# Performance work log

Measured on AMD Instinct MI355X. Metric: run time of the kernel, lower is better.

Reference implementation:

```python
import jax, jax.numpy as jnp
import numpy as np

D_MODEL = 128
D_STATE = 16
D_CONV = 2
EXPAND = 2
D_INNER = EXPAND * D_MODEL  # 256
DT_RANK = (D_MODEL + 15) // 16  # 8
GROUPS = 4
EPS = 1e-5


def setup_inputs() -> dict:
    key = jax.random.key(0)
    ks = jax.random.split(key, 12)
    s = lambda k, shape, sc=0.02: jax.random.normal(k, shape, dtype=jnp.float32) * sc
    inp = {
        "x_hsi": jax.random.normal(ks[0], (8, D_MODEL, 64, 64), dtype=jnp.float32),
        "W_in": s(ks[1], (D_MODEL, 2 * D_INNER)),            # in_proj (no bias)
        "conv_w": s(ks[2], (D_INNER, D_CONV), 0.5),          # depthwise causal conv, k=2
        "conv_b": s(ks[3], (D_INNER,), 0.1),
        "W_x": s(ks[4], (D_INNER, DT_RANK + 2 * D_STATE)),   # x_proj (no bias)
        "W_dt": s(ks[5], (DT_RANK, D_INNER), 0.1),
        "b_dt": s(ks[6], (D_INNER,), 0.1),
        "A_log": jnp.log(jnp.broadcast_to(jnp.arange(1, D_STATE + 1, dtype=jnp.float32), (D_INNER, D_STATE))),
        "D": jnp.ones((D_INNER,), dtype=jnp.float32),
        "W_out": s(ks[7], (D_INNER, D_MODEL)),               # out_proj (no bias)
        "gn_gamma": jnp.ones((D_MODEL,), dtype=jnp.float32),
        "gn_beta": jnp.zeros((D_MODEL,), dtype=jnp.float32),
    }
    return inp


def _causal_conv_k2(x, w, b):
    # x: [B, L, Din]; w: [Din, 2]; causal depthwise conv, kernel size 2
    xp = jnp.pad(x, ((0, 0), (1, 0), (0, 0)))
    return xp[:, :-1] * w[:, 0] + xp[:, 1:] * w[:, 1] + b


def _selective_scan(xc, dt, Bmat, Cmat, A, D):
    # xc,dt: [B,L,Din]; Bmat,Cmat: [B,L,N]; A: [Din,N]; D: [Din]
    def step(h, inp):
        dt_t, B_t, C_t, x_t = inp          # [B,Din],[B,N],[B,N],[B,Din]
        dA = jnp.exp(dt_t[..., None] * A)                      # [B,Din,N]
        dBx = dt_t[..., None] * B_t[:, None, :] * x_t[..., None]
        h = dA * h + dBx
        y = jnp.einsum('bdn,bn->bd', h, C_t)
        return h, y

    B_, L, Din = xc.shape
    h0 = jnp.zeros((B_, Din, A.shape[1]), dtype=xc.dtype)
    xs = (jnp.swapaxes(dt, 0, 1), jnp.swapaxes(Bmat, 0, 1),
          jnp.swapaxes(Cmat, 0, 1), jnp.swapaxes(xc, 0, 1))
    _, ys = jax.lax.scan(step, h0, xs)     # ys: [L,B,Din]
    return jnp.swapaxes(ys, 0, 1) + xc * D


def _mamba(x, W_in, conv_w, conv_b, W_x, W_dt, b_dt, A_log, D, W_out):
    # x: [B, L, d_model]
    xz = x @ W_in                                   # [B,L,2*Din]
    xh, z = jnp.split(xz, 2, axis=-1)
    xh = jax.nn.silu(_causal_conv_k2(xh, conv_w, conv_b))
    x_dbl = xh @ W_x                                # [B,L,dt_rank+2N]
    dt_low = x_dbl[..., :DT_RANK]
    Bmat = x_dbl[..., DT_RANK:DT_RANK + D_STATE]
    Cmat = x_dbl[..., DT_RANK + D_STATE:]
    dt = jax.nn.softplus(dt_low @ W_dt + b_dt)      # [B,L,Din]
    A = -jnp.exp(A_log)
    y = _selective_scan(xh, dt, Bmat, Cmat, A, D)
    y = y * jax.nn.silu(z)
    return y @ W_out


def _group_norm(x, gamma, beta):
    # x: [B,C,H,W]
    B_, C, H, W = x.shape
    xr = x.reshape(B_, GROUPS, -1)
    mean = xr.mean(-1, keepdims=True)
    var = xr.var(-1, keepdims=True)
    xn = ((xr - mean) * jax.lax.rsqrt(var + EPS)).reshape(B_, C, H, W)
    return xn * gamma[:, None, None] + beta[:, None, None]


def reference(x_hsi, W_in, conv_w, conv_b, W_x, W_dt, b_dt, A_log, D, W_out, gn_gamma, gn_beta):
    B_, C, H, W = x_hsi.shape
    x = jnp.transpose(x_hsi, (0, 2, 3, 1)).reshape(B_, H * W, C)
    x = _mamba(x, W_in, conv_w, conv_b, W_x, W_dt, b_dt, A_log, D, W_out)
    x = jnp.transpose(x.reshape(B_, H, W, C), (0, 3, 1, 2))
    x = jax.nn.silu(_group_norm(x, gn_gamma, gn_beta))
    return x + x_hsi
```

## Files before the change

kernel.cpp:

```cpp
#include <hip/hip_runtime.h>
#include <hip/hip_bf16.h>
#include <hip/hip_fp16.h>
#include <math.h>

#define BATCH   8
#define LSEQ    4096
#define CMODEL  128
#define DIN     256
#define NSTATE  16
#define RRANK   8
#define NCH     64
#define TCH     64

typedef __attribute__((ext_vector_type(8))) short short8;
typedef __attribute__((ext_vector_type(4))) float f32x4;
typedef __attribute__((ext_vector_type(2))) float f32x2;

__device__ __forceinline__ float sigmoid_fast(float x) {
    return __builtin_amdgcn_rcpf(1.0f + __expf(-x));
}
__device__ __forceinline__ float silu_fast(float x) { return x * sigmoid_fast(x); }
__device__ __forceinline__ float softplus_fast(float x) {
    return fmaxf(x, 0.0f) + __logf(1.0f + __expf(-fabsf(x)));
}
__device__ __forceinline__ float bf2f(unsigned short u) {
    return __uint_as_float(((unsigned)u) << 16);
}
__device__ __forceinline__ unsigned pk2bf(float a, float b) {
    __hip_bfloat162 t = __float22bfloat162_rn(make_float2(a, b));
    unsigned r;
    __builtin_memcpy(&r, &t, 4);
    return r;
}
__device__ __forceinline__ unsigned short f2bf1(float v) {
    return (unsigned short)pk2bf(v, v);
}
__device__ __forceinline__ f32x2 up2(unsigned w) {
    return (f32x2){ __uint_as_float(w << 16), __uint_as_float(w & 0xffff0000u) };
}

__device__ __forceinline__ void dA_powers2(float dtv, const float* A, bool fast,
                                           f32x2* dA2)
{
    if (fast) {
        float e1 = __expf(dtv * A[0]);
        float e2 = e1 * e1;
        dA2[0] = (f32x2){e1, e2};
        f32x2 e2s = (f32x2){e2, e2};
        #pragma unroll
        for (int j = 1; j < 8; ++j) dA2[j] = dA2[j-1] * e2s;
    } else {
        #pragma unroll
        for (int j = 0; j < 8; ++j)
            dA2[j] = (f32x2){__expf(dtv * A[2*j]), __expf(dtv * A[2*j+1])};
    }
}

#define LSTR 72

__device__ __forceinline__ void tr64_bf(const float* __restrict__ src, int lds,
                                        int r0, int c0,
                                        unsigned short* __restrict__ dst, int ldd)
{
    __shared__ float ts[64][65];
    const int tid = threadIdx.x;
    #pragma unroll
    for (int it = 0; it < 4; ++it) {
        int slot = tid + it * 256;
        int i = slot >> 4, j4 = slot & 15;
        float4 v = *(const float4*)&src[(size_t)(r0 + i) * lds + c0 + j4 * 4];
        ts[i][j4*4+0] = v.x; ts[i][j4*4+1] = v.y;
        ts[i][j4*4+2] = v.z; ts[i][j4*4+3] = v.w;
    }
    __syncthreads();
    #pragma unroll
    for (int it = 0; it < 4; ++it) {
        int slot = tid + it * 256;
        int row = slot >> 4, c4 = slot & 15;
        unsigned p0 = pk2bf(ts[c4*4+0][row], ts[c4*4+1][row]);
        unsigned p1 = pk2bf(ts[c4*4+2][row], ts[c4*4+3][row]);
        unsigned long long u = (unsigned long long)p0 | ((unsigned long long)p1 << 32);
        *(unsigned long long*)&dst[(size_t)(c0 + row) * ldd + r0 + c4 * 4] = u;
    }
}

__global__ __launch_bounds__(256) void k0_setup(
    const float* __restrict__ W_in, const float* __restrict__ W_out,
    unsigned short* __restrict__ wtin, unsigned short* __restrict__ wtout,
    float* __restrict__ part)
{
    const int bid = blockIdx.x;
    if (bid < 16) {
        int ct = bid >> 3, jt = bid & 7;
        tr64_bf(W_in, 512, ct * 64, jt * 64, wtin, 128);
    } else if (bid < 24) {
        int t3 = bid - 16;
        int kt = t3 >> 1, ct = t3 & 1;
        tr64_bf(W_out, 128, kt * 64, ct * 64, wtout, 256);
    } else {
        if (threadIdx.x < 64) part[threadIdx.x] = 0.0f;
    }
}

__global__ __launch_bounds__(512) void k1_gemm_in(
    const float* __restrict__ x_hsi, const unsigned short* __restrict__ wtin,
    unsigned short* __restrict__ xhbf, unsigned short* __restrict__ zbf)
{
    __shared__ __align__(16) unsigned short Abf[128 * LSTR];
    __shared__ __align__(16) unsigned short Bbf[256 * LSTR];
    const int tid = threadIdx.x;
    const int R0  = blockIdx.x * 128;
    const int b   = R0 >> 12;
    const int l0  = R0 & 4095;
    const int jbase = blockIdx.y * 256;

    const int w    = tid >> 6;
    const int lane = tid & 63;
    const int lm   = lane & 15;
    const int q    = lane >> 4;
    const int mbase = (w & 1) * 64;
    const int nbase = (w >> 1) * 64;

    f32x4 acc[4][4];
    #pragma unroll
    for (int i = 0; i < 4; ++i)
        #pragma unroll
        for (int j = 0; j < 4; ++j) acc[i][j] = (f32x4){0.f, 0.f, 0.f, 0.f};

    const int cq = tid & 15;
    const int lq = tid >> 4;

    for (int kc = 0; kc < 128; kc += 64) {
        __syncthreads();
        {
            float v[4][4];
            #pragma unroll
            for (int t = 0; t < 4; ++t) {
                float4 f = *(const float4*)&x_hsi[((b * 128 + kc + cq * 4 + t) << 12) + l0 + lq * 4];
                v[t][0] = f.x; v[t][1] = f.y; v[t][2] = f.z; v[t][3] = f.w;
            }
            #pragma unroll
            for (int i = 0; i < 4; ++i) {
                unsigned p0 = pk2bf(v[0][i], v[1][i]);
                unsigned p1 = pk2bf(v[2][i], v[3][i]);
                unsigned long long u = (unsigned long long)p0 | ((unsigned long long)p1 << 32);
                *(unsigned long long*)&Abf[(lq * 4 + i) * LSTR + cq * 4] = u;
            }
        }
        #pragma unroll
        for (int it = 0; it < 4; ++it) {
            int slot = tid + it * 512;
            int r = slot >> 3, seg = slot & 7;
            short8 vb = *(const short8*)&wtin[(size_t)(jbase + r) * 128 + kc + seg * 8];
            *(short8*)&Bbf[r * LSTR + seg * 8] = vb;
        }
        __syncthreads();
        #pragma unroll
        for (int kt = 0; kt < 2; ++kt) {
            short8 af[4], bfr[4];
            #pragma unroll
            for (int mt = 0; mt < 4; ++mt)
                af[mt] = *(const short8*)&Abf[(mbase + mt * 16 + lm) * LSTR + kt * 32 + q * 8];
            #pragma unroll
            for (int nt = 0; nt < 4; ++nt)
                bfr[nt] = *(const short8*)&Bbf[(nbase + nt * 16 + lm) * LSTR + kt * 32 + q * 8];
            #pragma unroll
            for (int mt = 0; mt < 4; ++mt)
                #pragma unroll
                for (int nt = 0; nt < 4; ++nt)
                    acc[mt][nt] = __builtin_amdgcn_mfma_f32_16x16x32_bf16(
                        af[mt], bfr[nt], acc[mt][nt], 0, 0, 0);
        }
    }

    const bool is_xh = (jbase == 0);
    #pragma unroll
    for (int mt = 0; mt < 4; ++mt) {
        #pragma unroll
        for (int r = 0; r < 4; ++r) {
            int row = R0 + mbase + mt * 16 + q * 4 + r;
            #pragma unroll
            for (int nt = 0; nt < 4; ++nt) {
                int col = nbase + nt * 16 + lm;
                float val = acc[mt][nt][r];
                if (is_xh) xhbf[row * 256 + col] = f2bf1(val);
                else       zbf[row * 256 + col]  = f2bf1(silu_fast(val));
            }
        }
    }
}

__global__ __launch_bounds__(256) void k4_xdbl(
    const unsigned short* __restrict__ xhbf, const float* __restrict__ conv_w,
    const float* __restrict__ conv_b, const float* __restrict__ W_x,
    float* __restrict__ xdbl, unsigned short* __restrict__ xcbf)
{
    __shared__ float xcs[64][68];
    __shared__ float wxs[64 * 40];
    __shared__ float cw0[256], cw1[256], cbs[256];
    const int tid = threadIdx.x;
    cw0[tid] = conv_w[2 * tid];
    cw1[tid] = conv_w[2 * tid + 1];
    cbs[tid] = conv_b[tid];

    const int R0 = blockIdx.x * 64;
    const int tc = tid & 7;
    const int tr = tid >> 3;

    float acc[2][5];
    #pragma unroll
    for (int i = 0; i < 2; ++i)
        #pragma unroll
        for (int j = 0; j < 5; ++j) acc[i][j] = 0.0f;

    for (int kc = 0; kc < 256; kc += 64) {
        __syncthreads();
        #pragma unroll
        for (int it = 0; it < 3; ++it) {
            int i4 = tid + it * 256;
            if (i4 < 640) ((float4*)wxs)[i4] = ((const float4*)&W_x[kc * 40])[i4];
        }
        #pragma unroll
        for (int it = 0; it < 4; ++it) {
            int idx = tid + it * 256;
            int r = idx >> 4, qq = idx & 15;
            int row = R0 + r;
            ushort4 cu = *(const ushort4*)&xhbf[(size_t)row * 256 + kc + qq * 4];
            float cur[4] = {bf2f(cu.x), bf2f(cu.y), bf2f(cu.z), bf2f(cu.w)};
            float pv[4] = {0.f, 0.f, 0.f, 0.f};
            if ((row & 4095) != 0) {
                ushort4 pu = *(const ushort4*)&xhbf[(size_t)(row - 1) * 256 + kc + qq * 4];
                pv[0] = bf2f(pu.x); pv[1] = bf2f(pu.y);
                pv[2] = bf2f(pu.z); pv[3] = bf2f(pu.w);
            }
            int d = kc + qq * 4;
            float o[4];
            #pragma unroll
            for (int e = 0; e < 4; ++e)
                o[e] = silu_fast(pv[e] * cw0[d+e] + cur[e] * cw1[d+e] + cbs[d+e]);
            *(float4*)&xcs[r][qq * 4] = make_float4(o[0], o[1], o[2], o[3]);
            unsigned p0 = pk2bf(o[0], o[1]), p1 = pk2bf(o[2], o[3]);
            unsigned long long u = (unsigned long long)p0 | ((unsigned long long)p1 << 32);
            *(unsigned long long*)&xcbf[(size_t)row * 256 + d] = u;
        }
        __syncthreads();
        #pragma unroll 2
        for (int k = 0; k < 64; ++k) {
            float wv[5];
            #pragma unroll
            for (int j = 0; j < 5; ++j) wv[j] = wxs[k * 40 + tc * 5 + j];
            #pragma unroll
            for (int i = 0; i < 2; ++i) {
                float a = xcs[tr * 2 + i][k];
                #pragma unroll
                for (int j = 0; j < 5; ++j) acc[i][j] = fmaf(a, wv[j], acc[i][j]);
            }
        }
    }
    #pragma unroll
    for (int i = 0; i < 2; ++i) {
        int row = R0 + tr * 2 + i;
        #pragma unroll
        for (int j = 0; j < 5; ++j) xdbl[row * 40 + tc * 5 + j] = acc[i][j];
    }
}

__global__ __launch_bounds__(256) void k6_scan1(
    const unsigned short* __restrict__ xcbf, const float* __restrict__ xdbl,
    const float* __restrict__ W_dt, const float* __restrict__ b_dt,
    const float* __restrict__ A_log,
    float* __restrict__ hend, float* __restrict__ dtsg)
{
    __shared__ __align__(16) unsigned char xdb[TCH * 64];
    const int d = threadIdx.x;
    const int chunk = blockIdx.x;
    const int b = blockIdx.y;
    const int t0 = b * LSEQ + chunk * TCH;

    #pragma unroll
    for (int it = 0; it < 2; ++it) {
        int slot = d + it * 256;
        int row = slot >> 3, seg = slot & 7;
        const float4* src = (const float4*)&xdbl[(size_t)(t0 + row) * 40];
        if (seg < 2) {
            *(float4*)&xdb[row * 64 + seg * 16] = src[seg];
        } else if (seg < 6) {
            float4 f = src[seg];
            unsigned p0 = pk2bf(f.x, f.y), p1 = pk2bf(f.z, f.w);
            *(uint2*)&xdb[row * 64 + 32 + (seg - 2) * 8] = make_uint2(p0, p1);
        }
    }

    float A[16];
    #pragma unroll
    for (int qq = 0; qq < 4; ++qq) {
        float4 al = *(const float4*)&A_log[d * 16 + qq * 4];
        A[qq*4+0] = -__expf(al.x); A[qq*4+1] = -__expf(al.y);
        A[qq*4+2] = -__expf(al.z); A[qq*4+3] = -__expf(al.w);
    }
    bool fast = true;
    #pragma unroll
    for (int n = 1; n < 16; ++n)
        fast = fast && (fabsf(A[n] - (n + 1) * A[0]) <= 1e-4f * fabsf(A[n]) + 1e-7f);

    float wdt[8];
    #pragma unroll
    for (int r = 0; r < 8; ++r) wdt[r] = W_dt[r * 256 + d];
    const float bdt = b_dt[d];

    f32x2 h2[8];
    #pragma unroll
    for (int j = 0; j < 8; ++j) h2[j] = (f32x2){0.f, 0.f};
    float dtsum = 0.f;
    __syncthreads();

    #pragma unroll 2
    for (int tt = 0; tt < TCH; ++tt) {
        const int row = t0 + tt;
        float xcv = bf2f(xcbf[(size_t)row * 256 + d]);

        const unsigned char* xr = &xdb[tt * 64];
        float dl[8];
        *(float4*)&dl[0] = *(const float4*)xr;
        *(float4*)&dl[4] = *(const float4*)(xr + 16);
        float dtr = bdt;
        #pragma unroll
        for (int r = 0; r < 8; ++r) dtr = fmaf(dl[r], wdt[r], dtr);
        float dtv = softplus_fast(dtr);
        dtsum += dtv;
        float dtx = dtv * xcv;

        uint4 bu0 = *(const uint4*)(xr + 32);
        uint4 bu1 = *(const uint4*)(xr + 48);
        f32x2 Bt2[8] = {up2(bu0.x), up2(bu0.y), up2(bu0.z), up2(bu0.w),
                        up2(bu1.x), up2(bu1.y), up2(bu1.z), up2(bu1.w)};

        f32x2 dA2[8];
        dA_powers2(dtv, A, fast, dA2);
        f32x2 dtx2 = (f32x2){dtx, dtx};
        #pragma unroll
        for (int j = 0; j < 8; ++j)
            h2[j] = dA2[j] * h2[j] + dtx2 * Bt2[j];
    }

    const float* hf = (const float*)h2;
    const int base = ((b * NCH + chunk) * 256 + d) * 16;
    #pragma unroll
    for (int qq = 0; qq < 4; ++qq)
        *(float4*)&hend[base + qq * 4] = make_float4(hf[qq*4], hf[qq*4+1], hf[qq*4+2], hf[qq*4+3]);
    dtsg[(b * NCH + chunk) * 256 + d] = dtsum;
}

__global__ __launch_bounds__(256) void k7_combine(
    const float* __restrict__ dtsg, const float* __restrict__ A_log,
    float* __restrict__ hx)
{
    const int idx = blockIdx.x * 256 + threadIdx.x;
    const int b = idx >> 12;
    const int rem = idx & 4095;
    const int d = rem >> 4, n = rem & 15;
    const float An = -__expf(A_log[d * 16 + n]);
    const int base = b * NCH * 4096 + rem;
    const int sbase = b * NCH * 256 + d;
    float h = 0.f;
    float Sb[8], Eb[8];
    #pragma unroll
    for (int j = 0; j < 8; ++j) {
        Sb[j] = dtsg[sbase + j * 256];
        Eb[j] = hx[base + j * 4096];
    }
    for (int g = 0; g < NCH / 8; ++g) {
        const int o  = base + g * 32768;
        const int so = sbase + g * 2048;
        float Sn[8] = {0,0,0,0,0,0,0,0}, En[8] = {0,0,0,0,0,0,0,0};
        if (g < NCH / 8 - 1) {
            #pragma unroll
            for (int j = 0; j < 8; ++j) {
                Sn[j] = dtsg[so + 2048 + j * 256];
                En[j] = hx[o + 32768 + j * 4096];
            }
        }
        #pragma unroll
        for (int j = 0; j < 8; ++j) {
            hx[o + j * 4096] = h;
            float P = __expf(Sb[j] * An);
            h = fmaf(P, h, Eb[j]);
        }
        #pragma unroll
        for (int j = 0; j < 8; ++j) { Sb[j] = Sn[j]; Eb[j] = En[j]; }
    }
}

__global__ __launch_bounds__(256) void k8_scan2(
    const unsigned short* __restrict__ xcbf, const float* __restrict__ xdbl,
    const float* __restrict__ W_dt, const float* __restrict__ b_dt,
    const float* __restrict__ A_log,
    const float* __restrict__ Dvec, const float* __restrict__ hin,
    const unsigned short* __restrict__ zbf, unsigned short* __restrict__ ybf)
{
    __shared__ __align__(16) unsigned char xdb[TCH * 96];
    const int d = threadIdx.x;
    const int chunk = blockIdx.x;
    const int b = blockIdx.y;
    const int t0 = b * LSEQ + chunk * TCH;

    #pragma unroll
    for (int it = 0; it < 2; ++it) {
        int slot = d + it * 256;
        int row = slot >> 3, s8 = slot & 7;
        float4 f = *(const float4*)&xdbl[(size_t)(t0 + row) * 40 + 8 + s8 * 4];
        unsigned p0 = pk2bf(f.x, f.y), p1 = pk2bf(f.z, f.w);
        *(uint2*)&xdb[row * 96 + 32 + s8 * 8] = make_uint2(p0, p1);
    }
    if (d < 128) {
        int row = d >> 1, seg = d & 1;
        *(float4*)&xdb[row * 96 + seg * 16] =
            *(const float4*)&xdbl[(size_t)(t0 + row) * 40 + seg * 4];
    }

    float A[16];
    #pragma unroll
    for (int qq = 0; qq < 4; ++qq) {
        float4 al = *(const float4*)&A_log[d * 16 + qq * 4];
        A[qq*4+0] = -__expf(al.x); A[qq*4+1] = -__expf(al.y);
        A[qq*4+2] = -__expf(al.z); A[qq*4+3] = -__expf(al.w);
    }
    bool fast = true;
    #pragma unroll
    for (int n = 1; n < 16; ++n)
        fast = fast && (fabsf(A[n] - (n + 1) * A[0]) <= 1e-4f * fabsf(A[n]) + 1e-7f);

    float wdt[8];
    #pragma unroll
    for (int r = 0; r < 8; ++r) wdt[r] = W_dt[r * 256 + d];
    const float bdt = b_dt[d];
    const float Dd = Dvec[d];

    f32x2 h2[8];
    const int hbase = ((b * NCH + chunk) * 256 + d) * 16;
    {
        float hf[16];
        #pragma unroll
        for (int qq = 0; qq < 4; ++qq) {
            float4 hv = *(const float4*)&hin[hbase + qq * 4];
            hf[qq*4+0] = hv.x; hf[qq*4+1] = hv.y; hf[qq*4+2] = hv.z; hf[qq*4+3] = hv.w;
        }
        #pragma unroll
        for (int j = 0; j < 8; ++j) h2[j] = (f32x2){hf[2*j], hf[2*j+1]};
    }
    __syncthreads();

    #pragma unroll 2
    for (int tt = 0; tt < TCH; ++tt) {
        const int row = t0 + tt;
        const size_t gi = (size_t)row * 256 + d;
        float xcv = bf2f(xcbf[gi]);

        const unsigned char* xr = &xdb[tt * 96];
        float dl[8];
        *(float4*)&dl[0] = *(const float4*)xr;
        *(float4*)&dl[4] = *(const float4*)(xr + 16);
        float dtr = bdt;
        #pragma unroll
        for (int r = 0; r < 8; ++r) dtr = fmaf(dl[r], wdt[r], dtr);
        float dtv = softplus_fast(dtr);
        float dtx = dtv * xcv;

        uint4 bu0 = *(const uint4*)(xr + 32);
        uint4 bu1 = *(const uint4*)(xr + 48);
        uint4 cu0 = *(const uint4*)(xr + 64);
        uint4 cu1 = *(const uint4*)(xr + 80);
        f32x2 Bt2[8] = {up2(bu0.x), up2(bu0.y), up2(bu0.z), up2(bu0.w),
                        up2(bu1.x), up2(bu1.y), up2(bu1.z), up2(bu1.w)};
        f32x2 Ct2[8] = {up2(cu0.x), up2(cu0.y), up2(cu0.z), up2(cu0.w),
                        up2(cu1.x), up2(cu1.y), up2(cu1.z), up2(cu1.w)};

        f32x2 dA2[8];
        dA_powers2(dtv, A, fast, dA2);
        f32x2 dtx2 = (f32x2){dtx, dtx};
        f32x2 yv2 = (f32x2){0.f, 0.f};
        #pragma unroll
        for (int j = 0; j < 8; ++j) {
            h2[j] = dA2[j] * h2[j] + dtx2 * Bt2[j];
            yv2 = yv2 + h2[j] * Ct2[j];
        }
        float yv = yv2.x + yv2.y;
        yv = fmaf(Dd, xcv, yv);
        ybf[gi] = f2bf1(yv * bf2f(zbf[gi]));
    }
}

__global__ __launch_bounds__(256) void k9_gemm_out(
    const unsigned short* __restrict__ ybf, const unsigned short* __restrict__ wtout,
    unsigned short* __restrict__ out_bf, float* __restrict__ part)
{
    __shared__ __align__(16) unsigned short Abf[128 * LSTR];
    __shared__ __align__(16) unsigned short Bbf[64 * LSTR];
    __shared__ float pred[8];
    const int tid = threadIdx.x;
    const int R0 = blockIdx.x * 64;
    const int b  = R0 >> 12;
    const int l0 = R0 & 4095;

    const int w    = tid >> 6;
    const int lane = tid & 63;
    const int lm   = lane & 15;
    const int q    = lane >> 4;
    const int mbase = (w & 1) * 64;
    const int nbase = (w >> 1) * 32;

    if (tid < 8) pred[tid] = 0.0f;

    f32x4 acc[4][2];
    #pragma unroll
    for (int i = 0; i < 4; ++i)
        #pragma unroll
        for (int j = 0; j < 2; ++j) acc[i][j] = (f32x4){0.f, 0.f, 0.f, 0.f};

    for (int kc = 0; kc < 256; kc += 64) {
        __syncthreads();
        #pragma unroll
        for (int it = 0; it < 4; ++it) {
            int slot = tid + it * 256;
            int r = slot >> 3, seg = slot & 7;
            short8 va = *(const short8*)&wtout[(size_t)r * 256 + kc + seg * 8];
            *(short8*)&Abf[r * LSTR + seg * 8] = va;
        }
        #pragma unroll
        for (int it = 0; it < 2; ++it) {
            int slot = tid + it * 256;
            int r = slot >> 3, seg = slot & 7;
            short8 vb = *(const short8*)&ybf[(size_t)(R0 + r) * 256 + kc + seg * 8];
            *(short8*)&Bbf[r * LSTR + seg * 8] = vb;
        }
        __syncthreads();
        #pragma unroll
        for (int kt = 0; kt < 2; ++kt) {
            short8 af[4], bfr[2];
            #pragma unroll
            for (int mt = 0; mt < 4; ++mt)
                af[mt] = *(const short8*)&Abf[(mbase + mt * 16 + lm) * LSTR + kt * 32 + q * 8];
            #pragma unroll
            for (int nt = 0; nt < 2; ++nt)
                bfr[nt] = *(const short8*)&Bbf[(nbase + nt * 16 + lm) * LSTR + kt * 32 + q * 8];
            #pragma unroll
            for (int mt = 0; mt < 4; ++mt)
                #pragma unroll
                for (int nt = 0; nt < 2; ++nt)
                    acc[mt][nt] = __builtin_amdgcn_mfma_f32_16x16x32_bf16(
                        af[mt], bfr[nt], acc[mt][nt], 0, 0, 0);
        }
    }

    #pragma unroll
    for (int mt = 0; mt < 4; ++mt) {
        #pragma unroll
        for (int r = 0; r < 4; ++r) {
            int c = mbase + mt * 16 + q * 4 + r;
            long base = (long)(b * 128 + c) * 4096 + l0;
            #pragma unroll
            for (int nt = 0; nt < 2; ++nt)
                out_bf[base + nbase + nt * 16 + lm] = f2bf1(acc[mt][nt][r]);
        }
    }

    float s0 = 0.f, q0 = 0.f, s1 = 0.f, q1 = 0.f;
    #pragma unroll
    for (int mt = 0; mt < 4; ++mt)
        #pragma unroll
        for (int nt = 0; nt < 2; ++nt)
            #pragma unroll
            for (int r = 0; r < 4; ++r) {
                float v = acc[mt][nt][r];
                if (mt < 2) { s0 += v; q0 += v * v; }
                else        { s1 += v; q1 += v * v; }
            }
    #pragma unroll
    for (int off = 32; off > 0; off >>= 1) {
        s0 += __shfl_down(s0, off, 64);
        q0 += __shfl_down(q0, off, 64);
        s1 += __shfl_down(s1, off, 64);
        q1 += __shfl_down(q1, off, 64);
    }
    if (lane == 0) {
        int g0 = mbase >> 5;
        atomicAdd(&pred[g0 * 2],           s0);
        atomicAdd(&pred[g0 * 2 + 1],       q0);
        atomicAdd(&pred[(g0 + 1) * 2],     s1);
        atomicAdd(&pred[(g0 + 1) * 2 + 1], q1);
    }
    __syncthreads();
    if (tid < 8) atomicAdd(&part[b * 8 + tid], pred[tid]);
}

__global__ __launch_bounds__(256) void k10c_apply(
    const unsigned short* __restrict__ out_bf, const float* __restrict__ part,
    const float* __restrict__ gamma, const float* __restrict__ beta,
    const float* __restrict__ x_hsi, float* __restrict__ out)
{
    __shared__ float sstat[64];
    if (threadIdx.x < 32) {
        float S = part[threadIdx.x * 2];
        float Q = part[threadIdx.x * 2 + 1];
        const float inv_n = 1.0f / 131072.0f;
        float mean = S * inv_n;
        float var  = Q * inv_n - mean * mean;
        sstat[threadIdx.x * 2]     = mean;
        sstat[threadIdx.x * 2 + 1] = rsqrtf(var + 1e-5f);
    }
    __syncthreads();
    const int idx4 = blockIdx.x * 256 + threadIdx.x;
    const int flat = idx4 * 4;
    const int c = (flat >> 12) & 127;
    const int b = flat >> 19;
    const int g = c >> 5;
    const float mean = sstat[(b * 4 + g) * 2];
    const float inv  = sstat[(b * 4 + g) * 2 + 1];
    const float ga = gamma[c], be = beta[c];
    ushort4 u = *(const ushort4*)&out_bf[flat];
    float4 r = *(const float4*)&x_hsi[flat];
    float vv[4] = {bf2f(u.x), bf2f(u.y), bf2f(u.z), bf2f(u.w)};
    float rr[4] = {r.x, r.y, r.z, r.w};
    float o[4];
    #pragma unroll
    for (int qq = 0; qq < 4; ++qq) {
        float xn = (vv[qq] - mean) * inv;
        float gv = xn * ga + be;
        o[qq] = silu_fast(gv) + rr[qq];
    }
    *(float4*)&out[flat] = make_float4(o[0], o[1], o[2], o[3]);
}

extern "C" void kernel_launch(void* const* d_in, const int* in_sizes, int n_in,
                              void* d_out, int out_size, void* d_ws, size_t ws_size,
                              hipStream_t stream)
{
    const float* x_hsi  = (const float*)d_in[0];
    const float* W_in   = (const float*)d_in[1];
    const float* conv_w = (const float*)d_in[2];
    const float* conv_b = (const float*)d_in[3];
    const float* W_x    = (const float*)d_in[4];
    const float* W_dt   = (const float*)d_in[5];
    const float* b_dt   = (const float*)d_in[6];
    const float* A_log  = (const float*)d_in[7];
    const float* Dv     = (const float*)d_in[8];
    const float* W_out  = (const float*)d_in[9];
    const float* gnw    = (const float*)d_in[10];
    const float* gnb    = (const float*)d_in[11];

    float* ws = (float*)d_ws;
    unsigned short* xhbf = (unsigned short*)(ws + 0);
    unsigned short* zbf  = (unsigned short*)(ws + 4194304);
    float* xdbl   = ws + 8388608;
    float* hx     = ws + 8716288;
    float* dtsg   = ws + 10813440;
    unsigned short* xcbf   = (unsigned short*)(ws + 10944512);
    unsigned short* out_bf = (unsigned short*)(ws + 15138816);
    float* part   = ws + 17235968;
    unsigned short* wtin  = (unsigned short*)(ws + 17236032);
    unsigned short* wtout = (unsigned short*)(ws + 17268800);
    unsigned short* ybf   = xhbf;
    float* outp   = (float*)d_out;

    k0_setup<<<25, 256, 0, stream>>>(W_in, W_out, wtin, wtout, part);
    k1_gemm_in<<<dim3(256, 2), 512, 0, stream>>>(x_hsi, wtin, xhbf, zbf);
    k4_xdbl<<<512, 256, 0, stream>>>(xhbf, conv_w, conv_b, W_x, xdbl, xcbf);
    k6_scan1<<<dim3(NCH, BATCH), 256, 0, stream>>>(xcbf, xdbl, W_dt, b_dt, A_log,
                                                   hx, dtsg);
    k7_combine<<<128, 256, 0, stream>>>(dtsg, A_log, hx);
    k8_scan2<<<dim3(NCH, BATCH), 256, 0, stream>>>(xcbf, xdbl, W_dt, b_dt, A_log,
                                                   Dv, hx, zbf, ybf);
    k9_gemm_out<<<512, 256, 0, stream>>>(ybf, wtout, out_bf, part);
    k10c_apply<<<4096, 256, 0, stream>>>(out_bf, part, gnw, gnb, x_hsi, outp);
}
```

Measured before the change: 215.3 us.

## Fuse conv+x_proj with scan pass 1, and scan pass 2 with out_proj GEMM

Merges the conv/x_proj kernel into the first chunked scan kernel, keeping xc and x_dbl in LDS and using fp32 B values instead of bf16. Also merges the second scan pass with the output projection GEMM, so the gated y tile stays in LDS rather than going through global memory. This removes two launches and the y round trip through global memory. The cost is more LDS per block (around 34KB for the y tile), which lowers occupancy, and a 512-block grid where each block runs a serial scan.

```diff
diff --git a/kernel.cpp b/kernel.cpp
--- a/kernel.cpp
+++ b/kernel.cpp
@@ -35,9 +35,6 @@
 __device__ __forceinline__ unsigned short f2bf1(float v) {
     return (unsigned short)pk2bf(v, v);
 }
-__device__ __forceinline__ f32x2 up2(unsigned w) {
-    return (f32x2){ __uint_as_float(w << 16), __uint_as_float(w & 0xffff0000u) };
-}
 
 __device__ __forceinline__ void dA_powers2(float dtv, const float* A, bool fast,
                                            f32x2* dA2)
@@ -57,6 +54,7 @@
 }
 
 #define LSTR 72
+#define YSTR 264
 
 __device__ __forceinline__ void tr64_bf(const float* __restrict__ src, int lds,
                                         int r0, int c0,
@@ -190,20 +188,44 @@
     }
 }
 
-__global__ __launch_bounds__(256) void k4_xdbl(
+__global__ __launch_bounds__(256) void k46_conv_gemm_scan1(
     const unsigned short* __restrict__ xhbf, const float* __restrict__ conv_w,
     const float* __restrict__ conv_b, const float* __restrict__ W_x,
-    float* __restrict__ xdbl, unsigned short* __restrict__ xcbf)
+    const float* __restrict__ W_dt, const float* __restrict__ b_dt,
+    const float* __restrict__ A_log,
+    float* __restrict__ xdbl, unsigned short* __restrict__ xcbf,
+    float* __restrict__ hend, float* __restrict__ dtsg)
 {
     __shared__ float xcs[64][68];
-    __shared__ float wxs[64 * 40];
+    __shared__ __align__(16) float wxs[64 * 40];
     __shared__ float cw0[256], cw1[256], cbs[256];
+    __shared__ __align__(16) unsigned short xcb[64][YSTR];
     const int tid = threadIdx.x;
+    const int chunk = blockIdx.x;
+    const int b = blockIdx.y;
+    const int R0 = b * LSEQ + chunk * TCH;
+
     cw0[tid] = conv_w[2 * tid];
     cw1[tid] = conv_w[2 * tid + 1];
     cbs[tid] = conv_b[tid];
 
-    const int R0 = blockIdx.x * 64;
+    const int d = tid;
+    float A[16];
+    #pragma unroll
+    for (int qq = 0; qq < 4; ++qq) {
+        float4 al = *(const float4*)&A_log[d * 16 + qq * 4];
+        A[qq*4+0] = -__expf(al.x); A[qq*4+1] = -__expf(al.y);
+        A[qq*4+2] = -__expf(al.z); A[qq*4+3] = -__expf(al.w);
+    }
+    bool fast = true;
+    #pragma unroll
+    for (int n = 1; n < 16; ++n)
+        fast = fast && (fabsf(A[n] - (n + 1) * A[0]) <= 1e-4f * fabsf(A[n]) + 1e-7f);
+    float wdt[8];
+    #pragma unroll
+    for (int r = 0; r < 8; ++r) wdt[r] = W_dt[r * 256 + d];
+    const float bdt = b_dt[d];
+
     const int tc = tid & 7;
     const int tr = tid >> 3;
 
@@ -233,15 +255,16 @@
                 pv[0] = bf2f(pu.x); pv[1] = bf2f(pu.y);
                 pv[2] = bf2f(pu.z); pv[3] = bf2f(pu.w);
             }
-            int d = kc + qq * 4;
+            int dd = kc + qq * 4;
             float o[4];
             #pragma unroll
             for (int e = 0; e < 4; ++e)
-                o[e] = silu_fast(pv[e] * cw0[d+e] + cur[e] * cw1[d+e] + cbs[d+e]);
+                o[e] = silu_fast(pv[e] * cw0[dd+e] + cur[e] * cw1[dd+e] + cbs[dd+e]);
             *(float4*)&xcs[r][qq * 4] = make_float4(o[0], o[1], o[2], o[3]);
             unsigned p0 = pk2bf(o[0], o[1]), p1 = pk2bf(o[2], o[3]);
             unsigned long long u = (unsigned long long)p0 | ((unsigned long long)p1 << 32);
-            *(unsigned long long*)&xcbf[(size_t)row * 256 + d] = u;
+            *(unsigned long long*)&xcb[r][dd] = u;
+            *(unsigned long long*)&xcbf[(size_t)row * 256 + dd] = u;
         }
         __syncthreads();
         #pragma unroll 2
@@ -257,72 +280,33 @@
             }
         }
     }
+
+    __syncthreads();
+    float* xdl = wxs;
     #pragma unroll
     for (int i = 0; i < 2; ++i) {
-        int row = R0 + tr * 2 + i;
-        #pragma unroll
-        for (int j = 0; j < 5; ++j) xdbl[row * 40 + tc * 5 + j] = acc[i][j];
-    }
-}
-
-__global__ __launch_bounds__(256) void k6_scan1(
-    const unsigned short* __restrict__ xcbf, const float* __restrict__ xdbl,
-    const float* __restrict__ W_dt, const float* __restrict__ b_dt,
-    const float* __restrict__ A_log,
-    float* __restrict__ hend, float* __restrict__ dtsg)
-{
-    __shared__ __align__(16) unsigned char xdb[TCH * 64];
-    const int d = threadIdx.x;
-    const int chunk = blockIdx.x;
-    const int b = blockIdx.y;
-    const int t0 = b * LSEQ + chunk * TCH;
-
-    #pragma unroll
-    for (int it = 0; it < 2; ++it) {
-        int slot = d + it * 256;
-        int row = slot >> 3, seg = slot & 7;
-        const float4* src = (const float4*)&xdbl[(size_t)(t0 + row) * 40];
-        if (seg < 2) {
-            *(float4*)&xdb[row * 64 + seg * 16] = src[seg];
-        } else if (seg < 6) {
-            float4 f = src[seg];
-            unsigned p0 = pk2bf(f.x, f.y), p1 = pk2bf(f.z, f.w);
-            *(uint2*)&xdb[row * 64 + 32 + (seg - 2) * 8] = make_uint2(p0, p1);
-        }
-    }
-
-    float A[16];
-    #pragma unroll
-    for (int qq = 0; qq < 4; ++qq) {
-        float4 al = *(const float4*)&A_log[d * 16 + qq * 4];
-        A[qq*4+0] = -__expf(al.x); A[qq*4+1] = -__expf(al.y);
-        A[qq*4+2] = -__expf(al.z); A[qq*4+3] = -__expf(al.w);
-    }
-    bool fast = true;
-    #pragma unroll
-    for (int n = 1; n < 16; ++n)
-        fast = fast && (fabsf(A[n] - (n + 1) * A[0]) <= 1e-4f * fabsf(A[n]) + 1e-7f);
-
-    float wdt[8];
-    #pragma unroll
-    for (int r = 0; r < 8; ++r) wdt[r] = W_dt[r * 256 + d];
-    const float bdt = b_dt[d];
+        int row = tr * 2 + i;
+        #pragma unroll
+        for (int j = 0; j < 5; ++j) {
+            float v = acc[i][j];
+            xdl[row * 40 + tc * 5 + j] = v;
+            xdbl[(size_t)(R0 + row) * 40 + tc * 5 + j] = v;
+        }
+    }
+    __syncthreads();
 
     f32x2 h2[8];
     #pragma unroll
     for (int j = 0; j < 8; ++j) h2[j] = (f32x2){0.f, 0.f};
     float dtsum = 0.f;
-    __syncthreads();
 
     #pragma unroll 2
     for (int tt = 0; tt < TCH; ++tt) {
-        const int row = t0 + tt;
-        float xcv = bf2f(xcbf[(size_t)row * 256 + d]);
-
-        const unsigned char* xr = &xdb[tt * 64];
+        float xcv = bf2f(xcb[tt][d]);
+
         float dl[8];
-        *(float4*)&dl[0] = *(const float4*)xr;
-        *(float4*)&dl[4] = *(const float4*)(xr + 16);
+        *(float4*)&dl[0] = *(const float4*)&xdl[tt * 40 + 0];
+        *(float4*)&dl[4] = *(const float4*)&xdl[tt * 40 + 4];
         float dtr = bdt;
         #pragma unroll
         for (int r = 0; r < 8; ++r) dtr = fmaf(dl[r], wdt[r], dtr);
@@ -330,17 +314,20 @@
         dtsum += dtv;
         float dtx = dtv * xcv;
 
-        uint4 bu0 = *(const uint4*)(xr + 32);
-        uint4 bu1 = *(const uint4*)(xr + 48);
-        f32x2 Bt2[8] = {up2(bu0.x), up2(bu0.y), up2(bu0.z), up2(bu0.w),
-                        up2(bu1.x), up2(bu1.y), up2(bu1.z), up2(bu1.w)};
+        float Bv[16];
+        *(float4*)&Bv[0]  = *(const float4*)&xdl[tt * 40 + 8];
+        *(float4*)&Bv[4]  = *(const float4*)&xdl[tt * 40 + 12];
+        *(float4*)&Bv[8]  = *(const float4*)&xdl[tt * 40 + 16];
+        *(float4*)&Bv[12] = *(const float4*)&xdl[tt * 40 + 20];
 
         f32x2 dA2[8];
         dA_powers2(dtv, A, fast, dA2);
         f32x2 dtx2 = (f32x2){dtx, dtx};
         #pragma unroll
-        for (int j = 0; j < 8; ++j)
-            h2[j] = dA2[j] * h2[j] + dtx2 * Bt2[j];
+        for (int j = 0; j < 8; ++j) {
+            f32x2 Bt2 = (f32x2){Bv[2*j], Bv[2*j+1]};
+            h2[j] = dA2[j] * h2[j] + dtx2 * Bt2;
+        }
     }
 
     const float* hf = (const float*)h2;
@@ -391,33 +378,31 @@
     }
 }
 
-__global__ __launch_bounds__(256) void k8_scan2(
+__global__ __launch_bounds__(256) void k89_scan2_gemm_out(
     const unsigned short* __restrict__ xcbf, const float* __restrict__ xdbl,
     const float* __restrict__ W_dt, const float* __restrict__ b_dt,
-    const float* __restrict__ A_log,
-    const float* __restrict__ Dvec, const float* __restrict__ hin,
-    const unsigned short* __restrict__ zbf, unsigned short* __restrict__ ybf)
-{
-    __shared__ __align__(16) unsigned char xdb[TCH * 96];
-    const int d = threadIdx.x;
+    const float* __restrict__ A_log, const float* __restrict__ Dvec,
+    const float* __restrict__ hin, const unsigned short* __restrict__ zbf,
+    const unsigned short* __restrict__ wtout,
+    unsigned short* __restrict__ out_bf, float* __restrict__ part)
+{
+    __shared__ __align__(16) float xdb[TCH * 40];
+    __shared__ __align__(16) unsigned short Ybf[64][YSTR];
+    __shared__ __align__(16) unsigned short Abf[128 * LSTR];
+    __shared__ float pred[8];
+    const int tid = threadIdx.x;
     const int chunk = blockIdx.x;
     const int b = blockIdx.y;
     const int t0 = b * LSEQ + chunk * TCH;
 
     #pragma unroll
-    for (int it = 0; it < 2; ++it) {
-        int slot = d + it * 256;
-        int row = slot >> 3, s8 = slot & 7;
-        float4 f = *(const float4*)&xdbl[(size_t)(t0 + row) * 40 + 8 + s8 * 4];
-        unsigned p0 = pk2bf(f.x, f.y), p1 = pk2bf(f.z, f.w);
-        *(uint2*)&xdb[row * 96 + 32 + s8 * 8] = make_uint2(p0, p1);
-    }
-    if (d < 128) {
-        int row = d >> 1, seg = d & 1;
-        *(float4*)&xdb[row * 96 + seg * 16] =
-            *(const float4*)&xdbl[(size_t)(t0 + row) * 40 + seg * 4];
-    }
-
+    for (int it = 0; it < 3; ++it) {
+        int i4 = tid + it * 256;
+        if (i4 < 640) ((float4*)xdb)[i4] = ((const float4*)&xdbl[(size_t)t0 * 40])[i4];
+    }
+    if (tid < 8) pred[tid] = 0.0f;
+
+    const int d = tid;
     float A[16];
     #pragma unroll
     for (int qq = 0; qq < 4; ++qq) {
@@ -429,7 +414,6 @@
     #pragma unroll
     for (int n = 1; n < 16; ++n)
         fast = fast && (fabsf(A[n] - (n + 1) * A[0]) <= 1e-4f * fabsf(A[n]) + 1e-7f);
-
     float wdt[8];
     #pragma unroll
     for (int r = 0; r < 8; ++r) wdt[r] = W_dt[r * 256 + d];
@@ -437,8 +421,8 @@
     const float Dd = Dvec[d];
 
     f32x2 h2[8];
-    const int hbase = ((b * NCH + chunk) * 256 + d) * 16;
     {
+        const int hbase = ((b * NCH + chunk) * 256 + d) * 16;
         float hf[16];
         #pragma unroll
         for (int qq = 0; qq < 4; ++qq) {
@@ -452,28 +436,27 @@
 
     #pragma unroll 2
     for (int tt = 0; tt < TCH; ++tt) {
-        const int row = t0 + tt;
-        const size_t gi = (size_t)row * 256 + d;
+        const size_t gi = (size_t)(t0 + tt) * 256 + d;
         float xcv = bf2f(xcbf[gi]);
 
-        const unsigned char* xr = &xdb[tt * 96];
         float dl[8];
-        *(float4*)&dl[0] = *(const float4*)xr;
-        *(float4*)&dl[4] = *(const float4*)(xr + 16);
+        *(float4*)&dl[0] = *(const float4*)&xdb[tt * 40 + 0];
+        *(float4*)&dl[4] = *(const float4*)&xdb[tt * 40 + 4];
         float dtr = bdt;
         #pragma unroll
         for (int r = 0; r < 8; ++r) dtr = fmaf(dl[r], wdt[r], dtr);
         float dtv = softplus_fast(dtr);
         float dtx = dtv * xcv;
 
-        uint4 bu0 = *(const uint4*)(xr + 32);
-        uint4 bu1 = *(const uint4*)(xr + 48);
-        uint4 cu0 = *(const uint4*)(xr + 64);
-        uint4 cu1 = *(const uint4*)(xr + 80);
-        f32x2 Bt2[8] = {up2(bu0.x), up2(bu0.y), up2(bu0.z), up2(bu0.w),
-                        up2(bu1.x), up2(bu1.y), up2(bu1.z), up2(bu1.w)};
-        f32x2 Ct2[8] = {up2(cu0.x), up2(cu0.y), up2(cu0.z), up2(cu0.w),
-                        up2(cu1.x), up2(cu1.y), up2(cu1.z), up2(cu1.w)};
+        float Bv[16], Cv[16];
+        *(float4*)&Bv[0]  = *(const float4*)&xdb[tt * 40 + 8];
+        *(float4*)&Bv[4]  = *(const float4*)&xdb[tt * 40 + 12];
+        *(float4*)&Bv[8]  = *(const float4*)&xdb[tt * 40 + 16];
+        *(float4*)&Bv[12] = *(const float4*)&xdb[tt * 40 + 20];
+        *(float4*)&Cv[0]  = *(const float4*)&xdb[tt * 40 + 24];
+        *(float4*)&Cv[4]  = *(const float4*)&xdb[tt * 40 + 28];
+        *(float4*)&Cv[8]  = *(const float4*)&xdb[tt * 40 + 32];
+        *(float4*)&Cv[12] = *(const float4*)&xdb[tt * 40 + 36];
 
         f32x2 dA2[8];
         dA_powers2(dtv, A, fast, dA2);
@@ -481,26 +464,15 @@
         f32x2 yv2 = (f32x2){0.f, 0.f};
         #pragma unroll
         for (int j = 0; j < 8; ++j) {
-            h2[j] = dA2[j] * h2[j] + dtx2 * Bt2[j];
-            yv2 = yv2 + h2[j] * Ct2[j];
+            f32x2 Bt2 = (f32x2){Bv[2*j], Bv[2*j+1]};
+            f32x2 Ct2 = (f32x2){Cv[2*j], Cv[2*j+1]};
+            h2[j] = dA2[j] * h2[j] + dtx2 * Bt2;
+            yv2 = yv2 + h2[j] * Ct2;
         }
         float yv = yv2.x + yv2.y;
         yv = fmaf(Dd, xcv, yv);
-        ybf[gi] = f2bf1(yv * bf2f(zbf[gi]));
-    }
-}
-
-__global__ __launch_bounds__(256) void k9_gemm_out(
-    const unsigned short* __restrict__ ybf, const unsigned short* __restrict__ wtout,
-    unsigned short* __restrict__ out_bf, float* __restrict__ part)
-{
-    __shared__ __align__(16) unsigned short Abf[128 * LSTR];
-    __shared__ __align__(16) unsigned short Bbf[64 * LSTR];
-    __shared__ float pred[8];
-    const int tid = threadIdx.x;
-    const int R0 = blockIdx.x * 64;
-    const int b  = R0 >> 12;
-    const int l0 = R0 & 4095;
+        Ybf[tt][d] = f2bf1(yv * bf2f(zbf[gi]));
+    }
 
     const int w    = tid >> 6;
     const int lane = tid & 63;
@@ -509,8 +481,6 @@
     const int mbase = (w & 1) * 64;
     const int nbase = (w >> 1) * 32;
 
-    if (tid < 8) pred[tid] = 0.0f;
-
     f32x4 acc[4][2];
     #pragma unroll
     for (int i = 0; i < 4; ++i)
@@ -526,13 +496,6 @@
             short8 va = *(const short8*)&wtout[(size_t)r * 256 + kc + seg * 8];
             *(short8*)&Abf[r * LSTR + seg * 8] = va;
         }
-        #pragma unroll
-        for (int it = 0; it < 2; ++it) {
-            int slot = tid + it * 256;
-            int r = slot >> 3, seg = slot & 7;
-            short8 vb = *(const short8*)&ybf[(size_t)(R0 + r) * 256 + kc + seg * 8];
-            *(short8*)&Bbf[r * LSTR + seg * 8] = vb;
-        }
         __syncthreads();
         #pragma unroll
         for (int kt = 0; kt < 2; ++kt) {
@@ -542,7 +505,7 @@
                 af[mt] = *(const short8*)&Abf[(mbase + mt * 16 + lm) * LSTR + kt * 32 + q * 8];
             #pragma unroll
             for (int nt = 0; nt < 2; ++nt)
-                bfr[nt] = *(const short8*)&Bbf[(nbase + nt * 16 + lm) * LSTR + kt * 32 + q * 8];
+                bfr[nt] = *(const short8*)&Ybf[nbase + nt * 16 + lm][kc + kt * 32 + q * 8];
             #pragma unroll
             for (int mt = 0; mt < 4; ++mt)
                 #pragma unroll
@@ -552,15 +515,16 @@
         }
     }
 
+    const int l0 = chunk * TCH;
     #pragma unroll
     for (int mt = 0; mt < 4; ++mt) {
         #pragma unroll
         for (int r = 0; r < 4; ++r) {
             int c = mbase + mt * 16 + q * 4 + r;
-            long base = (long)(b * 128 + c) * 4096 + l0;
+            long obase = (long)(b * 128 + c) * 4096 + l0;
             #pragma unroll
             for (int nt = 0; nt < 2; ++nt)
-                out_bf[base + nbase + nt * 16 + lm] = f2bf1(acc[mt][nt][r]);
+                out_bf[obase + nbase + nt * 16 + lm] = f2bf1(acc[mt][nt][r]);
         }
     }
 
@@ -659,17 +623,14 @@
     float* part   = ws + 17235968;
     unsigned short* wtin  = (unsigned short*)(ws + 17236032);
     unsigned short* wtout = (unsigned short*)(ws + 17268800);
-    unsigned short* ybf   = xhbf;
     float* outp   = (float*)d_out;
 
     k0_setup<<<25, 256, 0, stream>>>(W_in, W_out, wtin, wtout, part);
     k1_gemm_in<<<dim3(256, 2), 512, 0, stream>>>(x_hsi, wtin, xhbf, zbf);
-    k4_xdbl<<<512, 256, 0, stream>>>(xhbf, conv_w, conv_b, W_x, xdbl, xcbf);
-    k6_scan1<<<dim3(NCH, BATCH), 256, 0, stream>>>(xcbf, xdbl, W_dt, b_dt, A_log,
-                                                   hx, dtsg);
+    k46_conv_gemm_scan1<<<dim3(NCH, BATCH), 256, 0, stream>>>(
+        xhbf, conv_w, conv_b, W_x, W_dt, b_dt, A_log, xdbl, xcbf, hx, dtsg);
     k7_combine<<<128, 256, 0, stream>>>(dtsg, A_log, hx);
-    k8_scan2<<<dim3(NCH, BATCH), 256, 0, stream>>>(xcbf, xdbl, W_dt, b_dt, A_log,
-                                                   Dv, hx, zbf, ybf);
-    k9_gemm_out<<<512, 256, 0, stream>>>(ybf, wtout, out_bf, part);
+    k89_scan2_gemm_out<<<dim3(NCH, BATCH), 256, 0, stream>>>(
+        xcbf, xdbl, W_dt, b_dt, A_log, Dv, hx, zbf, wtout, out_bf, part);
     k10c_apply<<<4096, 256, 0, stream>>>(out_bf, part, gnw, gnb, x_hsi, outp);
 }
```

Result: faster. 196.1 us (-9.0%).
